# Kernel optimization log

Measured on AMD Instinct MI355X. Metric: run time of the kernel, lower is better.

The kernel has to match this reference:

```python
import jax, jax.numpy as jnp
import numpy as np

V = 5023          # FLAME vertex count
NJ = 5            # joints: global, neck, jaw, eyeL, eyeR
N_SHAPE = 100
N_EXP = 50
PARENTS = np.array([-1, 0, 1, 1, 1], dtype=np.int64)  # static kintree
N_BATCH = 2048


def setup_inputs() -> dict:
    key = jax.random.key(0)
    ks = jax.random.split(key, 12)
    N = N_BATCH
    shape = jax.random.normal(ks[0], (N, N_SHAPE), jnp.float32)
    exp = jax.random.normal(ks[1], (N, N_EXP), jnp.float32)
    neck_pose = 0.1 * jax.random.normal(ks[2], (N, 3), jnp.float32)
    jaw_pose = 0.1 * jax.random.normal(ks[3], (N, 3), jnp.float32)
    eye_pose = 0.1 * jax.random.normal(ks[4], (N, 6), jnp.float32)
    v_template = jax.random.normal(ks[5], (V, 3), jnp.float32)
    shapedirs = 0.01 * jax.random.normal(ks[6], (V, 3, N_SHAPE + N_EXP), jnp.float32)
    posedirs = 0.01 * jax.random.normal(ks[7], (36, V * 3), jnp.float32)
    J_regressor = jax.random.uniform(ks[8], (NJ, V), jnp.float32)
    J_regressor = J_regressor / J_regressor.sum(axis=1, keepdims=True)
    lbs_weights = jax.random.uniform(ks[9], (V, NJ), jnp.float32)
    lbs_weights = lbs_weights / lbs_weights.sum(axis=1, keepdims=True)
    parents = jnp.asarray(PARENTS)
    return dict(shape=shape, exp=exp, neck_pose=neck_pose, jaw_pose=jaw_pose,
                eye_pose=eye_pose, v_template=v_template, shapedirs=shapedirs,
                posedirs=posedirs, J_regressor=J_regressor, lbs_weights=lbs_weights,
                parents=parents)


def rodrigues(rot_vecs):
    """Axis-angle [...,3] -> rotation matrices [...,3,3] (matches SMPL/FLAME impl)."""
    angle = jnp.linalg.norm(rot_vecs + 1e-8, axis=-1, keepdims=True)
    rd = rot_vecs / angle
    cos = jnp.cos(angle)[..., None]
    sin = jnp.sin(angle)[..., None]
    rx, ry, rz = rd[..., 0], rd[..., 1], rd[..., 2]
    z = jnp.zeros_like(rx)
    K = jnp.stack([z, -rz, ry, rz, z, -rx, -ry, rx, z], axis=-1).reshape(rd.shape + (3,))
    I = jnp.eye(3, dtype=rot_vecs.dtype)
    return I + sin * K + (1.0 - cos) * (K @ K)


def flame_forward(shape, exp, neck_pose, jaw_pose, eye_pose, v_template,
                  shapedirs, posedirs, J_regressor, lbs_weights):
    N = shape.shape[0]
    dt = shape.dtype
    betas = jnp.concatenate([shape, exp], axis=1)                      # [N,150]
    # full pose: zeroed global rot + neck + jaw + eyes -> [N,NJ,3]
    full_pose = jnp.concatenate([jnp.zeros_like(jaw_pose), neck_pose,
                                 jaw_pose, eye_pose], axis=1).reshape(N, NJ, 3)
    # shape blendshapes
    v_shaped = v_template[None] + jnp.einsum('bl,vkl->bvk', betas, shapedirs)  # [N,V,3]
    J = jnp.einsum('jv,bvk->bjk', J_regressor, v_shaped)               # [N,NJ,3]
    # pose blendshapes
    R = rodrigues(full_pose)                                           # [N,NJ,3,3]
    pose_feature = (R[:, 1:] - jnp.eye(3, dtype=dt)).reshape(N, (NJ - 1) * 9)
    v_posed = v_shaped + (pose_feature @ posedirs).reshape(N, V, 3)
    # kinematic chain (static 5-joint tree)
    rel_J = J.at[:, 1:].add(-J[:, PARENTS[1:]])
    Rt = jnp.concatenate([R, rel_J[..., None]], axis=-1)               # [N,NJ,3,4]
    bottom = jnp.broadcast_to(jnp.array([0., 0., 0., 1.], dtype=dt), (N, NJ, 1, 4))
    T = jnp.concatenate([Rt, bottom], axis=2)                          # [N,NJ,4,4]
    chain = [T[:, 0]]
    for i in range(1, NJ):
        chain.append(chain[int(PARENTS[i])] @ T[:, i])
    G = jnp.stack(chain, axis=1)                                       # [N,NJ,4,4]
    # remove rest-pose joint locations from the transforms
    J_h = jnp.concatenate([J, jnp.zeros((N, NJ, 1), dt)], axis=-1)     # [N,NJ,4]
    t_corr = jnp.einsum('bjrc,bjc->bjr', G, J_h)
    A = G.at[..., 3].add(-t_corr)                                      # [N,NJ,4,4]
    # linear blend skinning
    Tw = jnp.einsum('vj,bjrc->bvrc', lbs_weights, A)                   # [N,V,4,4]
    v_h = jnp.concatenate([v_posed, jnp.ones((N, V, 1), dt)], axis=-1)
    verts = jnp.einsum('bvrc,bvc->bvr', Tw, v_h)[..., :3]              # [N,V,3]
    return verts


def reference(shape, exp, neck_pose, jaw_pose, eye_pose, v_template,
              shapedirs, posedirs, J_regressor, lbs_weights, parents):
    # parents is a static buffer (PARENTS) -- accepted for signature parity.
    return flame_forward(shape, exp, neck_pose, jaw_pose, eye_pose, v_template,
                         shapedirs, posedirs, J_regressor, lbs_weights)
```

## Files before the change

kernel.cpp:

```cpp
#include <hip/hip_runtime.h>
#include <hip/hip_bf16.h>
#include <math.h>

#define NV   5023
#define N3   15069
#define NB   2048
#define NTIL 79
#define NPAD (NTIL*192)

#define WS_JD_B   0
#define WS_ATR_B  9216
#define WS_AB_B   795648
#define WS_BB_B   1582080

typedef __attribute__((ext_vector_type(8))) short short8;
typedef __attribute__((ext_vector_type(4))) float floatx4;

static __device__ __forceinline__ unsigned short f2bf(float x) {
    union { __hip_bfloat16 h; unsigned short s; } u;
    u.h = __float2bfloat16(x);
    return u.s;
}
static __device__ __forceinline__ unsigned int pk2(float a, float b) {
    return (unsigned int)f2bf(a) | ((unsigned int)f2bf(b) << 16);
}

#define BAR_LGKM() do { \
    asm volatile("s_waitcnt lgkmcnt(0)" ::: "memory"); \
    __builtin_amdgcn_s_barrier(); \
    asm volatile("" ::: "memory"); \
} while (0)

__global__ void k_zero(char* ws) {
    int i = blockIdx.x * 256 + threadIdx.x;
    if (i < 2272) ((float*)(ws + WS_JD_B))[i] = 0.f;
}

__global__ void k_prep(const float* __restrict__ Jreg,
                       const float* __restrict__ sdirs,
                       const float* __restrict__ vt,
                       const float* __restrict__ pdirs,
                       char* __restrict__ ws) {
    if (blockIdx.x < 126) {
        int slice = blockIdx.x;
        int start = slice * 40;
        int end   = min(start + 40, NV);
        int t = threadIdx.x;
        int s0 = t, s1 = t + 256;
        float a0[5] = {0,0,0,0,0}, a1[5] = {0,0,0,0,0};
        for (int v = start; v < end; ++v) {
            float w[5];
            #pragma unroll
            for (int j = 0; j < 5; ++j) w[j] = Jreg[j * NV + v];
            float x0 = (s0 < 450) ? sdirs[(size_t)v * 450 + s0]
                     : (s0 < 453 ? vt[v * 3 + (s0 - 450)] : 0.f);
            float x1 = (s1 < 450) ? sdirs[(size_t)v * 450 + s1]
                     : (s1 < 453 ? vt[v * 3 + (s1 - 450)] : 0.f);
            #pragma unroll
            for (int j = 0; j < 5; ++j) { a0[j] += w[j] * x0; a1[j] += w[j] * x1; }
        }
        float* Jd = (float*)(ws + WS_JD_B);
        #pragma unroll
        for (int j = 0; j < 5; ++j) {
            if (s0 < 453) atomicAdd(&Jd[j * 453 + s0], a0[j]);
            if (s1 < 453) atomicAdd(&Jd[j * 453 + s1], a1[j]);
        }
    } else {
        int idx = (blockIdx.x - 126) * 256 + threadIdx.x;
        int kg = idx % 24, n = idx / 24;
        int k0 = kg * 8;
        __hip_bfloat16 val[8];
        #pragma unroll
        for (int e = 0; e < 8; ++e) {
            int k = k0 + e;
            float v = 0.f;
            if (n < N3) {
                if (k < 150)      v = sdirs[(size_t)n * 150 + k];
                else if (k < 186) v = pdirs[(size_t)(k - 150) * N3 + n];
            }
            val[e] = __float2bfloat16(v);
        }
        *(int4*)((__hip_bfloat16*)(ws + WS_BB_B) + (size_t)n * 192 + k0) = *(int4*)val;
    }
}

__global__ void k_batch(const float* __restrict__ shp,
                        const float* __restrict__ expn,
                        const float* __restrict__ neck,
                        const float* __restrict__ jaw,
                        const float* __restrict__ eye,
                        char* __restrict__ ws) {
    __shared__ float JdL[2265];
    {
        const float* Jd = (const float*)(ws + WS_JD_B);
        for (int i = threadIdx.x; i < 2265; i += 64) JdL[i] = Jd[i];
    }
    __syncthreads();
    int b = blockIdx.x * 64 + threadIdx.x;
    float* Atr = (float*)(ws + WS_ATR_B) + (size_t)b * 60;
    unsigned int* A32 = (unsigned int*)((char*)ws + WS_AB_B + (size_t)b * 384);

    float J[15];
    #pragma unroll
    for (int jk = 0; jk < 15; ++jk) J[jk] = JdL[(jk / 3) * 453 + 450 + (jk % 3)];

    for (int l4 = 0; l4 < 25; ++l4) {
        float4 be = *(const float4*)(shp + (size_t)b * 100 + l4 * 4);
        A32[2*l4]     = pk2(be.x, be.y);
        A32[2*l4 + 1] = pk2(be.z, be.w);
        float bev[4] = {be.x, be.y, be.z, be.w};
        #pragma unroll
        for (int e = 0; e < 4; ++e) {
            int l = l4 * 4 + e;
            #pragma unroll
            for (int jj = 0; jj < 5; ++jj)
                #pragma unroll
                for (int kk = 0; kk < 3; ++kk)
                    J[jj * 3 + kk] += JdL[jj * 453 + kk * 150 + l] * bev[e];
        }
    }
    for (int l2 = 0; l2 < 25; ++l2) {
        float2 be = *(const float2*)(expn + (size_t)b * 50 + l2 * 2);
        A32[50 + l2] = pk2(be.x, be.y);
        float bev[2] = {be.x, be.y};
        #pragma unroll
        for (int e = 0; e < 2; ++e) {
            int l = 100 + l2 * 2 + e;
            #pragma unroll
            for (int jj = 0; jj < 5; ++jj)
                #pragma unroll
                for (int kk = 0; kk < 3; ++kk)
                    J[jj * 3 + kk] += JdL[jj * 453 + kk * 150 + l] * bev[e];
        }
    }

    float R[5][9];
    for (int jj = 0; jj < 5; ++jj) {
        float rx, ry, rz;
        if (jj == 0)      { rx = 0.f; ry = 0.f; rz = 0.f; }
        else if (jj == 1) { rx = neck[b*3]; ry = neck[b*3+1]; rz = neck[b*3+2]; }
        else if (jj == 2) { rx = jaw[b*3];  ry = jaw[b*3+1];  rz = jaw[b*3+2];  }
        else if (jj == 3) { rx = eye[b*6];  ry = eye[b*6+1];  rz = eye[b*6+2];  }
        else              { rx = eye[b*6+3]; ry = eye[b*6+4]; rz = eye[b*6+5];  }
        float ax = rx + 1e-8f, ay = ry + 1e-8f, az = rz + 1e-8f;
        float angle = sqrtf(ax*ax + ay*ay + az*az);
        float inv = 1.f / angle;
        float ux = rx * inv, uy = ry * inv, uz = rz * inv;
        float c = cosf(angle), s = sinf(angle);
        float K[9] = {0.f, -uz, uy,  uz, 0.f, -ux,  -uy, ux, 0.f};
        float KK[9];
        #pragma unroll
        for (int r = 0; r < 3; ++r)
            #pragma unroll
            for (int cc = 0; cc < 3; ++cc) {
                float a = 0.f;
                #pragma unroll
                for (int m = 0; m < 3; ++m) a += K[r*3+m] * K[m*3+cc];
                KK[r*3+cc] = a;
            }
        #pragma unroll
        for (int e = 0; e < 9; ++e) R[jj][e] = s * K[e] + (1.f - c) * KK[e];
        R[jj][0] += 1.f; R[jj][4] += 1.f; R[jj][8] += 1.f;
    }

    float pf_loc[36];
    #pragma unroll
    for (int jj = 1; jj < 5; ++jj)
        #pragma unroll
        for (int e = 0; e < 9; ++e)
            pf_loc[(jj-1)*9 + e] = R[jj][e] - ((e == 0 || e == 4 || e == 8) ? 1.f : 0.f);
    #pragma unroll
    for (int i = 0; i < 18; ++i) A32[75 + i] = pk2(pf_loc[2*i], pf_loc[2*i + 1]);
    A32[93] = 0u; A32[94] = 0u; A32[95] = 0u;

    float G[5][12];
    #pragma unroll
    for (int r = 0; r < 3; ++r) {
        #pragma unroll
        for (int cc = 0; cc < 3; ++cc) G[0][r*4+cc] = R[0][r*3+cc];
        G[0][r*4+3] = J[r];
    }
    const int par[5] = {-1, 0, 1, 1, 1};
    for (int jj = 1; jj < 5; ++jj) {
        int p = par[jj];
        float rel[3];
        #pragma unroll
        for (int r = 0; r < 3; ++r) rel[r] = J[jj*3+r] - J[p*3+r];
        #pragma unroll
        for (int r = 0; r < 3; ++r) {
            #pragma unroll
            for (int cc = 0; cc < 3; ++cc) {
                float a = 0.f;
                #pragma unroll
                for (int m = 0; m < 3; ++m) a += G[p][r*4+m] * R[jj][m*3+cc];
                G[jj][r*4+cc] = a;
            }
            float tt = G[p][r*4+3];
            #pragma unroll
            for (int m = 0; m < 3; ++m) tt += G[p][r*4+m] * rel[m];
            G[jj][r*4+3] = tt;
        }
    }
    for (int jj = 0; jj < 5; ++jj)
        #pragma unroll
        for (int r = 0; r < 3; ++r) {
            float tc = 0.f;
            #pragma unroll
            for (int m = 0; m < 3; ++m) tc += G[jj][r*4+m] * J[jj*3+m];
            Atr[jj*12 + r*4 + 0] = G[jj][r*4+0];
            Atr[jj*12 + r*4 + 1] = G[jj][r*4+1];
            Atr[jj*12 + r*4 + 2] = G[jj][r*4+2];
            Atr[jj*12 + r*4 + 3] = G[jj][r*4+3] - tc;
        }
}

#define A_OFF  0
#define B_OFF  17408
#define S_VT   33
#define S_AT   61
#define VT_T_OFF 0
#define ATR_OFF  25344
#define VTQ_OFF  33152
#define LBS_OFF  33920
#define SMEM_BYTES 43520

__global__ __launch_bounds__(256, 3) void k_mega(
        const char* __restrict__ ws,
        const float* __restrict__ vt,
        const float* __restrict__ lbsw,
        float* __restrict__ out) {
    __shared__ __align__(16) unsigned char smem[SMEM_BYTES];
    const unsigned char* AbG = (const unsigned char*)ws + WS_AB_B;
    const unsigned char* BbG = (const unsigned char*)ws + WS_BB_B;
    const float* AtrG = (const float*)(ws + WS_ATR_B);

    const int ntile = blockIdx.y;
    const int b0    = blockIdx.x * 128;
    const int t     = threadIdx.x;
    const int lane  = t & 63;
    const int wn    = t >> 6;
    const int l15 = lane & 15, quad = lane >> 4;

    floatx4 acc[8][3];
    #pragma unroll
    for (int f = 0; f < 8; ++f)
        #pragma unroll
        for (int g = 0; g < 3; ++g) {
            floatx4 z = {0.f, 0.f, 0.f, 0.f};
            acc[f][g] = z;
        }

    for (int chunk = 0; chunk < 3; ++chunk) {
        __syncthreads();
        #pragma unroll
        for (int i = 0; i < 4; ++i) {
            int flat = i * 256 + t;
            int row = flat >> 3, piece = flat & 7;
            *(float4*)(smem + A_OFF + row * 136 + piece * 16) =
                *(const float4*)(AbG + (size_t)(b0 + row) * 384 + chunk * 128 + piece * 16);
        }
        #pragma unroll
        for (int i = 0; i < 6; ++i) {
            int flat = i * 256 + t;
            int row = flat >> 3, piece = flat & 7;
            *(float4*)(smem + B_OFF + row * 136 + piece * 16) =
                *(const float4*)(BbG + (size_t)(ntile * 192 + row) * 384 + chunk * 128 + piece * 16);
        }
        __syncthreads();
        #pragma unroll
        for (int ks = 0; ks < 2; ++ks) {
            short8 af[8];
            #pragma unroll
            for (int f = 0; f < 8; ++f)
                af[f] = *(const short8*)(smem + A_OFF + (f * 16 + l15) * 136 + ks * 64 + quad * 16);
            #pragma unroll
            for (int g = 0; g < 3; ++g) {
                short8 bf = *(const short8*)(smem + B_OFF + (wn * 48 + g * 16 + l15) * 136 + ks * 64 + quad * 16);
                #pragma unroll
                for (int f = 0; f < 8; ++f)
                    acc[f][g] = __builtin_amdgcn_mfma_f32_16x16x32_bf16(af[f], bf, acc[f][g], 0, 0, 0);
            }
        }
    }
    __syncthreads();

    float* vtT  = (float*)(smem + VT_T_OFF);
    float* atrS = (float*)(smem + ATR_OFF);
    float* vtQ  = (float*)(smem + VTQ_OFF);
    float* lbsS = (float*)(smem + LBS_OFF);

    if (t < 192) { int n = ntile * 192 + t; vtQ[t] = (n < N3) ? vt[n] : 0.f; }
    for (int i = t; i < 320; i += 256) {
        int v = ntile * 64 + i / 5;
        lbsS[i] = (v < NV) ? lbsw[(size_t)v * 5 + (i % 5)] : 0.f;
    }

    #pragma unroll
    for (int q = 0; q < 4; ++q) {
        BAR_LGKM();
        #pragma unroll
        for (int ff2 = 0; ff2 < 2; ++ff2) {
            int f = q * 2 + ff2;
            #pragma unroll
            for (int g = 0; g < 3; ++g) {
                int col = wn * 48 + g * 16 + l15;
                int rl  = ff2 * 16 + quad * 4;
                #pragma unroll
                for (int r = 0; r < 4; ++r)
                    vtT[col * S_VT + rl + r] = acc[f][g][r];
            }
        }
        for (int i = t; i < 1920; i += 256) {
            int rw = i / 60, cw = i - rw * 60;
            atrS[rw * S_AT + cw] = AtrG[((size_t)(b0 + q * 32)) * 60 + i];
        }
        BAR_LGKM();

        {
            int rl = t & 31;
            int vgrp = t >> 5;
            float ar[60];
            #pragma unroll
            for (int i = 0; i < 60; ++i) ar[i] = atrS[rl * S_AT + i];
            #pragma unroll
            for (int vv = 0; vv < 8; ++vv) {
                int vloc = vgrp * 8 + vv;
                int c0 = vloc * 3;
                float w0 = lbsS[vloc*5+0], w1 = lbsS[vloc*5+1], w2 = lbsS[vloc*5+2],
                      w3 = lbsS[vloc*5+3], w4 = lbsS[vloc*5+4];
                float px = vtT[(c0+0) * S_VT + rl] + vtQ[c0+0];
                float py = vtT[(c0+1) * S_VT + rl] + vtQ[c0+1];
                float pz = vtT[(c0+2) * S_VT + rl] + vtQ[c0+2];
                float y[3];
                #pragma unroll
                for (int r = 0; r < 3; ++r) {
                    float t0 = w0*ar[ 0+r*4+0] + w1*ar[12+r*4+0] + w2*ar[24+r*4+0]
                             + w3*ar[36+r*4+0] + w4*ar[48+r*4+0];
                    float t1 = w0*ar[ 0+r*4+1] + w1*ar[12+r*4+1] + w2*ar[24+r*4+1]
                             + w3*ar[36+r*4+1] + w4*ar[48+r*4+1];
                    float t2 = w0*ar[ 0+r*4+2] + w1*ar[12+r*4+2] + w2*ar[24+r*4+2]
                             + w3*ar[36+r*4+2] + w4*ar[48+r*4+2];
                    float t3 = w0*ar[ 0+r*4+3] + w1*ar[12+r*4+3] + w2*ar[24+r*4+3]
                             + w3*ar[36+r*4+3] + w4*ar[48+r*4+3];
                    y[r] = t0*px + t1*py + t2*pz + t3;
                }
                vtT[(c0+0) * S_VT + rl] = y[0];
                vtT[(c0+1) * S_VT + rl] = y[1];
                vtT[(c0+2) * S_VT + rl] = y[2];
            }
        }
        BAR_LGKM();
        {
            int wv = t >> 6;
            const bool full = (ntile * 192 + 192 <= N3);
            for (int rr = wv; rr < 32; rr += 4) {
                size_t ob = (size_t)(b0 + q * 32 + rr) * N3 + (size_t)ntile * 192;
                if (full) {
                    #pragma unroll
                    for (int e = 0; e < 3; ++e) {
                        int col = e * 64 + lane;
                        __builtin_nontemporal_store(vtT[col * S_VT + rr], &out[ob + col]);
                    }
                } else {
                    #pragma unroll
                    for (int e = 0; e < 3; ++e) {
                        int col = e * 64 + lane;
                        if (ntile * 192 + col < N3)
                            __builtin_nontemporal_store(vtT[col * S_VT + rr], &out[ob + col]);
                    }
                }
            }
        }
    }
}

extern "C" void kernel_launch(void* const* d_in, const int* in_sizes, int n_in,
                              void* d_out, int out_size, void* d_ws, size_t ws_size,
                              hipStream_t stream) {
    const float* shp  = (const float*)d_in[0];
    const float* expn = (const float*)d_in[1];
    const float* neck = (const float*)d_in[2];
    const float* jaw  = (const float*)d_in[3];
    const float* eye  = (const float*)d_in[4];
    const float* vt   = (const float*)d_in[5];
    const float* sdir = (const float*)d_in[6];
    const float* pdir = (const float*)d_in[7];
    const float* jreg = (const float*)d_in[8];
    const float* lbsw = (const float*)d_in[9];
    char* ws  = (char*)d_ws;
    float* out = (float*)d_out;

    k_zero <<<9,    256, 0, stream>>>(ws);
    k_prep <<<1548, 256, 0, stream>>>(jreg, sdir, vt, pdir, ws);
    k_batch<<<32,    64, 0, stream>>>(shp, expn, neck, jaw, eye, ws);
    k_mega <<<dim3(16, NTIL), 256, 0, stream>>>(ws, vt, lbsw, out);
}
```

Baseline: 281.6 us.

## Restructure prep packing with coalesced loads and halve mega-kernel batch tile

The prep kernel now stages J_regressor weights in shared memory, packs shapedirs to bf16 with vectorized float2 loads, and transposes posedirs through a shared-memory tile so global reads are coalesced. The main GEMM+skinning kernel uses a 64-row batch tile instead of 128, doubling the grid and cutting shared memory and accumulator registers. This should raise occupancy and parallelism, at the cost of reloading the B tile twice as often. The zeroing kernel is replaced by hipMemsetAsync.

```diff
diff --git a/kernel.cpp b/kernel.cpp
--- a/kernel.cpp
+++ b/kernel.cpp
@@ -13,6 +13,10 @@
 #define WS_AB_B   795648
 #define WS_BB_B   1582080
 
+#define GP_J 126
+#define GP_S 1067
+#define GP_P 237
+
 typedef __attribute__((ext_vector_type(8))) short short8;
 typedef __attribute__((ext_vector_type(4))) float floatx4;
 
@@ -31,33 +35,39 @@
     asm volatile("" ::: "memory"); \
 } while (0)
 
-__global__ void k_zero(char* ws) {
-    int i = blockIdx.x * 256 + threadIdx.x;
-    if (i < 2272) ((float*)(ws + WS_JD_B))[i] = 0.f;
-}
-
 __global__ void k_prep(const float* __restrict__ Jreg,
                        const float* __restrict__ sdirs,
                        const float* __restrict__ vt,
                        const float* __restrict__ pdirs,
                        char* __restrict__ ws) {
-    if (blockIdx.x < 126) {
+    __shared__ float JregL[200];
+    __shared__ float PL[36][65];
+    const int t = threadIdx.x;
+
+    if (blockIdx.x < GP_J) {
         int slice = blockIdx.x;
         int start = slice * 40;
         int end   = min(start + 40, NV);
-        int t = threadIdx.x;
+        if (t < 200) {
+            int j = t / 40, vl = t % 40;
+            int v = start + vl;
+            JregL[t] = (v < NV) ? Jreg[j * NV + v] : 0.f;
+        }
+        __syncthreads();
         int s0 = t, s1 = t + 256;
         float a0[5] = {0,0,0,0,0}, a1[5] = {0,0,0,0,0};
+        #pragma unroll 2
         for (int v = start; v < end; ++v) {
-            float w[5];
-            #pragma unroll
-            for (int j = 0; j < 5; ++j) w[j] = Jreg[j * NV + v];
+            int vl = v - start;
             float x0 = (s0 < 450) ? sdirs[(size_t)v * 450 + s0]
                      : (s0 < 453 ? vt[v * 3 + (s0 - 450)] : 0.f);
             float x1 = (s1 < 450) ? sdirs[(size_t)v * 450 + s1]
                      : (s1 < 453 ? vt[v * 3 + (s1 - 450)] : 0.f);
             #pragma unroll
-            for (int j = 0; j < 5; ++j) { a0[j] += w[j] * x0; a1[j] += w[j] * x1; }
+            for (int j = 0; j < 5; ++j) {
+                float w = JregL[j * 40 + vl];
+                a0[j] += w * x0; a1[j] += w * x1;
+            }
         }
         float* Jd = (float*)(ws + WS_JD_B);
         #pragma unroll
@@ -65,22 +75,55 @@
             if (s0 < 453) atomicAdd(&Jd[j * 453 + s0], a0[j]);
             if (s1 < 453) atomicAdd(&Jd[j * 453 + s1], a1[j]);
         }
+    } else if (blockIdx.x < GP_J + GP_S) {
+        int idx = (blockIdx.x - GP_J) * 256 + t;
+        if (idx < NPAD * 18) {
+            int n = idx / 18, g = idx % 18;
+            __hip_bfloat16* dst = (__hip_bfloat16*)(ws + WS_BB_B) + (size_t)n * 192 + g * 8;
+            if (n < N3) {
+                const float* src = sdirs + (size_t)n * 150 + g * 8;
+                float2 p0 = *(const float2*)(src);
+                float2 p1 = *(const float2*)(src + 2);
+                float2 p2 = *(const float2*)(src + 4);
+                float2 p3 = *(const float2*)(src + 6);
+                unsigned int w[4] = { pk2(p0.x, p0.y), pk2(p1.x, p1.y),
+                                      pk2(p2.x, p2.y), pk2(p3.x, p3.y) };
+                *(int4*)dst = *(int4*)w;
+            } else {
+                int4 z = {0, 0, 0, 0};
+                *(int4*)dst = z;
+            }
+        }
     } else {
-        int idx = (blockIdx.x - 126) * 256 + threadIdx.x;
-        int kg = idx % 24, n = idx / 24;
-        int k0 = kg * 8;
-        __hip_bfloat16 val[8];
-        #pragma unroll
-        for (int e = 0; e < 8; ++e) {
-            int k = k0 + e;
-            float v = 0.f;
-            if (n < N3) {
-                if (k < 150)      v = sdirs[(size_t)n * 150 + k];
-                else if (k < 186) v = pdirs[(size_t)(k - 150) * N3 + n];
-            }
-            val[e] = __float2bfloat16(v);
-        }
-        *(int4*)((__hip_bfloat16*)(ws + WS_BB_B) + (size_t)n * 192 + k0) = *(int4*)val;
+        int pb = blockIdx.x - (GP_J + GP_S);
+        int n0 = pb * 64;
+        #pragma unroll
+        for (int j = 0; j < 9; ++j) {
+            int flat = j * 256 + t;
+            int k = flat >> 6, i = flat & 63;
+            int n = n0 + i;
+            PL[k][i] = (n < N3) ? pdirs[(size_t)k * N3 + n] : 0.f;
+        }
+        __syncthreads();
+        #pragma unroll
+        for (int j = 0; j < 2; ++j) {
+            int idx2 = j * 256 + t;
+            if (idx2 < 384) {
+                int r = idx2 / 6, g = idx2 % 6;
+                int n = n0 + r;
+                int k0 = 144 + g * 8;
+                __hip_bfloat16 val[8];
+                #pragma unroll
+                for (int e = 0; e < 8; ++e) {
+                    int k = k0 + e;
+                    float v = 0.f;
+                    if (k < 150)      v = (n < N3) ? sdirs[(size_t)n * 150 + k] : 0.f;
+                    else if (k < 186) v = PL[k - 150][r];
+                    val[e] = __float2bfloat16(v);
+                }
+                *(int4*)((__hip_bfloat16*)(ws + WS_BB_B) + (size_t)n * 192 + k0) = *(int4*)val;
+            }
+        }
     }
 }
 
@@ -215,14 +258,14 @@
 }
 
 #define A_OFF  0
-#define B_OFF  17408
+#define B_OFF  8704
 #define S_VT   33
 #define S_AT   61
 #define VT_T_OFF 0
 #define ATR_OFF  25344
 #define VTQ_OFF  33152
 #define LBS_OFF  33920
-#define SMEM_BYTES 43520
+#define SMEM_BYTES 35200
 
 __global__ __launch_bounds__(256, 3) void k_mega(
         const char* __restrict__ ws,
@@ -235,15 +278,15 @@
     const float* AtrG = (const float*)(ws + WS_ATR_B);
 
     const int ntile = blockIdx.y;
-    const int b0    = blockIdx.x * 128;
+    const int b0    = blockIdx.x * 64;
     const int t     = threadIdx.x;
     const int lane  = t & 63;
     const int wn    = t >> 6;
     const int l15 = lane & 15, quad = lane >> 4;
 
-    floatx4 acc[8][3];
-    #pragma unroll
-    for (int f = 0; f < 8; ++f)
+    floatx4 acc[4][3];
+    #pragma unroll
+    for (int f = 0; f < 4; ++f)
         #pragma unroll
         for (int g = 0; g < 3; ++g) {
             floatx4 z = {0.f, 0.f, 0.f, 0.f};
@@ -253,7 +296,7 @@
     for (int chunk = 0; chunk < 3; ++chunk) {
         __syncthreads();
         #pragma unroll
-        for (int i = 0; i < 4; ++i) {
+        for (int i = 0; i < 2; ++i) {
             int flat = i * 256 + t;
             int row = flat >> 3, piece = flat & 7;
             *(float4*)(smem + A_OFF + row * 136 + piece * 16) =
@@ -269,15 +312,15 @@
         __syncthreads();
         #pragma unroll
         for (int ks = 0; ks < 2; ++ks) {
-            short8 af[8];
-            #pragma unroll
-            for (int f = 0; f < 8; ++f)
+            short8 af[4];
+            #pragma unroll
+            for (int f = 0; f < 4; ++f)
                 af[f] = *(const short8*)(smem + A_OFF + (f * 16 + l15) * 136 + ks * 64 + quad * 16);
             #pragma unroll
             for (int g = 0; g < 3; ++g) {
                 short8 bf = *(const short8*)(smem + B_OFF + (wn * 48 + g * 16 + l15) * 136 + ks * 64 + quad * 16);
                 #pragma unroll
-                for (int f = 0; f < 8; ++f)
+                for (int f = 0; f < 4; ++f)
                     acc[f][g] = __builtin_amdgcn_mfma_f32_16x16x32_bf16(af[f], bf, acc[f][g], 0, 0, 0);
             }
         }
@@ -296,7 +339,7 @@
     }
 
     #pragma unroll
-    for (int q = 0; q < 4; ++q) {
+    for (int q = 0; q < 2; ++q) {
         BAR_LGKM();
         #pragma unroll
         for (int ff2 = 0; ff2 < 2; ++ff2) {
@@ -390,8 +433,8 @@
     char* ws  = (char*)d_ws;
     float* out = (float*)d_out;
 
-    k_zero <<<9,    256, 0, stream>>>(ws);
-    k_prep <<<1548, 256, 0, stream>>>(jreg, sdir, vt, pdir, ws);
-    k_batch<<<32,    64, 0, stream>>>(shp, expn, neck, jaw, eye, ws);
-    k_mega <<<dim3(16, NTIL), 256, 0, stream>>>(ws, vt, lbsw, out);
-}
+    hipMemsetAsync(ws + WS_JD_B, 0, 2272 * 4, stream);
+    k_prep <<<GP_J + GP_S + GP_P, 256, 0, stream>>>(jreg, sdir, vt, pdir, ws);
+    k_batch<<<32, 64, 0, stream>>>(shp, expn, neck, jaw, eye, ws);
+    k_mega <<<dim3(32, NTIL), 256, 0, stream>>>(ws, vt, lbsw, out);
+}
```

Result: faster. 255.5 us (-9.3%).
